# Performance work log

Hardware: AMD Instinct MI355X
Metric: run time of the kernel (lower is better)

The kernel has to match this reference:

```python
import jax, jax.numpy as jnp
import numpy as np

B, T, E, VD, H = 1, 4096, 1024, 2048, 8
KD, HD = E // H, VD // H
EPS = 1e-6


def _make_rel_pos():
    # rotary angles: theta_i = 10000^(-2i/KD), repeated for even/odd pairs
    inv = 1.0 / (10000.0 ** (np.arange(0, KD, 2) / KD))
    angle = np.repeat(inv, 2)[None, :] * np.arange(T)[:, None]  # [T, KD]
    sin = jnp.asarray(np.sin(angle), dtype=jnp.float32)
    cos = jnp.asarray(np.cos(angle), dtype=jnp.float32)
    # per-head causal decay mask: gamma_h^(n-m) for n>=m else 0
    gamma = 1.0 - 2.0 ** (-5.0 - np.arange(H))  # [H]
    n = np.arange(T)
    diff = n[:, None] - n[None, :]  # [T, T]
    logg = np.log(gamma)[:, None, None]
    mask = np.where(diff[None] >= 0, np.exp(logg * np.maximum(diff[None], 0)), 0.0)
    return sin, cos, jnp.asarray(mask, dtype=jnp.float32)


def setup_inputs() -> dict:
    key = jax.random.key(0)
    ks = jax.random.split(key, 6)
    sin, cos, inner_mask = _make_rel_pos()
    s = lambda d: 1.0 / np.sqrt(d)
    return {
        "x": jax.random.normal(ks[0], (B, T, E), dtype=jnp.float32),
        "sin": sin,
        "cos": cos,
        "inner_mask": inner_mask,
        "Wq": jax.random.normal(ks[1], (E, E), dtype=jnp.float32) * s(E),
        "Wk": jax.random.normal(ks[2], (E, E), dtype=jnp.float32) * s(E),
        "Wv": jax.random.normal(ks[3], (E, VD), dtype=jnp.float32) * s(E),
        "Wg": jax.random.normal(ks[4], (E, VD), dtype=jnp.float32) * s(E),
        "Wo": jax.random.normal(ks[5], (VD, E), dtype=jnp.float32) * s(VD),
    }


def _rotate_every_two(x):
    x1 = x[..., ::2]
    x2 = x[..., 1::2]
    return jnp.stack((-x2, x1), axis=-1).reshape(x.shape)


def _theta_shift(x, sin, cos):
    return x * cos + _rotate_every_two(x) * sin


def reference(x, sin, cos, inner_mask, Wq, Wk, Wv, Wg, Wo):
    b, t, e = x.shape
    scaling = KD ** (-0.5)
    q = (x @ Wq).reshape(b, t, H, KD).transpose(0, 2, 1, 3)   # [b,h,t,kd]
    k = (x @ Wk * scaling).reshape(b, t, H, KD).transpose(0, 2, 1, 3)
    v = x @ Wv                                                # [b,t,vd]
    g = x @ Wg                                                # [b,t,vd]
    qr = _theta_shift(q, sin, cos)
    kr = _theta_shift(k, sin, cos)
    vr = v.reshape(b, t, H, HD).transpose(0, 2, 1, 3)         # [b,h,t,hd]
    qk = jnp.einsum('bhtd,bhsd->bhts', qr, kr) * inner_mask   # [b,h,t,t]
    denom = jnp.clip(jnp.abs(jax.lax.stop_gradient(qk)).sum(-1, keepdims=True), 1.0, 50000.0)
    qk = qk / denom
    out = jnp.einsum('bhts,bhsd->bhtd', qk, vr)               # [b,h,t,hd]
    out = out.transpose(0, 2, 1, 3)                           # [b,t,h,hd]
    # RMSNorm over head_dim, no affine
    out = out * jax.lax.rsqrt(jnp.mean(out * out, axis=-1, keepdims=True) + EPS)
    out = out.reshape(b, t, H * HD)
    out = jax.nn.silu(g) * out
    return out @ Wo
```

## Files before the change

kernel.cpp:

```cpp
#include <hip/hip_runtime.h>


typedef __attribute__((ext_vector_type(8)))  short  short8;
typedef __attribute__((ext_vector_type(16))) float  floatx16;

__device__ inline unsigned short f2bf(float f){
  unsigned int u = __builtin_bit_cast(unsigned int, f);
  unsigned int r = (u + 0x7fffu + ((u >> 16) & 1u)) >> 16;
  return (unsigned short)r;
}
__device__ inline float bf2f(unsigned short u){
  unsigned int x = ((unsigned int)u) << 16;
  return __builtin_bit_cast(float, x);
}
__device__ inline void async_cp16(const void* g, const void* l){
  __builtin_amdgcn_global_load_lds((const __attribute__((address_space(1))) void*)g,
                                   (__attribute__((address_space(3))) void*)l, 16, 0, 0);
}

struct us4 { unsigned short a,b,c,d; };
__global__ void k_cvt_x(const float* __restrict__ x, unsigned short* __restrict__ xb, int n4){
  int i = blockIdx.x*blockDim.x + threadIdx.x;
  if (i >= n4) return;
  float4 v = ((const float4*)x)[i];
  us4 o = { f2bf(v.x), f2bf(v.y), f2bf(v.z), f2bf(v.w) };
  ((us4*)xb)[i] = o;
}

struct WPrep  { const float* src; unsigned short* dst; int R; int C; int ntile; };
struct WPrepAll { WPrep w[5]; };
__global__ __launch_bounds__(256) void k_prep_w(WPrepAll a){
  __shared__ float tile[64][65];
  int b = blockIdx.x, i = 0;
  while (b >= a.w[i].ntile){ b -= a.w[i].ntile; ++i; }
  const float* src = a.w[i].src; unsigned short* dst = a.w[i].dst;
  int R = a.w[i].R, C = a.w[i].C;
  int tpr = C >> 6;
  int c0 = (b % tpr)*64, r0 = (b / tpr)*64;
  #pragma unroll
  for (int j=0;j<16;++j){
    int idx = j*256 + threadIdx.x; int r = idx>>6, c = idx&63;
    tile[r][c] = src[(size_t)(r0+r)*C + c0 + c];
  }
  __syncthreads();
  #pragma unroll
  for (int j=0;j<16;++j){
    int idx = j*256 + threadIdx.x; int r = idx>>6, c = idx&63;
    dst[(size_t)(c0+r)*R + r0 + c] = f2bf(tile[c][r]);
  }
}

__global__ __launch_bounds__(256) void k_transpose_b2b(const unsigned short* __restrict__ src,
    unsigned short* __restrict__ dst, int R, int C){
  __shared__ unsigned short tile[64][72];
  int c0 = blockIdx.x*64, r0 = blockIdx.y*64;
  #pragma unroll
  for (int i=0;i<16;++i){
    int idx = i*256 + threadIdx.x; int r = idx>>6, c = idx&63;
    tile[r][c] = src[(size_t)(r0+r)*C + c0 + c];
  }
  __syncthreads();
  #pragma unroll
  for (int i=0;i<16;++i){
    int idx = i*256 + threadIdx.x; int r = idx>>6, c = idx&63;
    dst[(size_t)(c0+r)*R + r0 + c] = tile[c][r];
  }
}

template<int MODE>
__global__ __launch_bounds__(256) void k_gemm_bt(
    const unsigned short* __restrict__ A, const unsigned short* __restrict__ BT,
    int M, int N, int K,
    float* __restrict__ out_f32, unsigned short* __restrict__ out_v,
    unsigned short* __restrict__ out_g)
{
  __shared__ __align__(16) short As[128*64];
  __shared__ __align__(16) short Bs[128*64];
  int bn = blockIdx.x*128, bm = blockIdx.y*128;
  int tid = threadIdx.x;
  int w = tid>>6, l = tid&63;
  int wr = w>>1, wc = w&1;
  int lrow = l&31, lhi = l>>5;
  floatx16 acc[2][2];
  #pragma unroll
  for (int a=0;a<2;++a)
    #pragma unroll
    for (int b=0;b<2;++b)
      #pragma unroll
      for (int j=0;j<16;++j) acc[a][b][j]=0.f;

  int kchunk = K / gridDim.z;
  int k_beg = blockIdx.z * kchunk;
  for (int k0=k_beg; k0<k_beg+kchunk; k0+=64){
    __syncthreads();
    #pragma unroll
    for (int i=0;i<4;++i){
      int idx = i*256 + tid; int r = idx>>3, c = idx&7;
      int cs = c ^ (r&7);
      async_cp16((const char*)A  + ((size_t)(bm+r)*K + k0 + cs*8)*2, &As[idx*8]);
      async_cp16((const char*)BT + ((size_t)(bn+r)*K + k0 + cs*8)*2, &Bs[idx*8]);
    }
    __syncthreads();
    #pragma unroll
    for (int kc=0;kc<4;++kc){
      short8 af[2], bf[2];
      #pragma unroll
      for (int tm=0;tm<2;++tm){
        int row = wr*64 + tm*32 + lrow;
        int pos = (2*kc + lhi) ^ (row&7);
        af[tm] = *(const short8*)&As[row*64 + pos*8];
      }
      #pragma unroll
      for (int tn=0;tn<2;++tn){
        int row = wc*64 + tn*32 + lrow;
        int pos = (2*kc + lhi) ^ (row&7);
        bf[tn] = *(const short8*)&Bs[row*64 + pos*8];
      }
      #pragma unroll
      for (int tm=0;tm<2;++tm)
        #pragma unroll
        for (int tn=0;tn<2;++tn)
          acc[tm][tn] = __builtin_amdgcn_mfma_f32_32x32x16_bf16(af[tm], bf[tn], acc[tm][tn], 0,0,0);
    }
  }
  #pragma unroll
  for (int tm=0;tm<2;++tm)
    #pragma unroll
    for (int tn=0;tn<2;++tn)
      #pragma unroll
      for (int r=0;r<16;++r){
        int row = bm + wr*64 + tm*32 + (r&3) + 8*(r>>2) + 4*lhi;
        int col = bn + wc*64 + tn*32 + lrow;
        float v = acc[tm][tn][r];
        if (MODE==0){
          if (col < 2048)      out_f32[(size_t)row*2048 + col] = v;
          else if (col < 4096) out_v[(size_t)row*2048 + (col-2048)] = f2bf(v);
          else                 out_g[(size_t)row*2048 + (col-4096)] = f2bf(v);
        } else {
          atomicAdd(&out_f32[(size_t)row*N + col], v);
        }
      }
}

__global__ void k_rotary(const float* __restrict__ qk, const float* __restrict__ sinp,
                         const float* __restrict__ cosp,
                         unsigned short* __restrict__ qrp, unsigned short* __restrict__ krp)
{
  int tid = blockIdx.x*blockDim.x + threadIdx.x;
  int t = tid >> 10, p = tid & 1023;
  bool isq = p < 512;
  int c = (isq ? p : p - 512)*2;
  int d = c & 127;
  const float* base = qk + (size_t)t*2048 + (isq ? 0 : 1024) + c;
  float f0 = base[0], f1 = base[1];
  float s0 = sinp[t*128 + d],   s1 = sinp[t*128 + d + 1];
  float c0 = cosp[t*128 + d],   c1 = cosp[t*128 + d + 1];
  float r0 = f0*c0 - f1*s0;
  float r1 = f1*c1 + f0*s1;
  if (!isq){ r0 *= 0.08838834764831845f; r1 *= 0.08838834764831845f; }
  unsigned short* dst = (isq ? qrp : krp) + (size_t)t*1024 + c;
  dst[0] = f2bf(r0); dst[1] = f2bf(r1);
}

__global__ __launch_bounds__(256, 2) void k_attn(
    const unsigned short* __restrict__ qr, const unsigned short* __restrict__ kr,
    const unsigned short* __restrict__ vT,
    unsigned short* __restrict__ o_acc0, unsigned short* __restrict__ o_acc1,
    float* __restrict__ den_g)
{
  int gid = blockIdx.x;
  int head = gid & 7;
  int rest = gid >> 3;
  int qt = 63 - (rest >> 1);
  int chunk = rest & 1;
  int tid = threadIdx.x;
  int w = tid>>6, l = tid&63;
  int qh = w>>1, hh = w&1;
  int lrow = l&31, lhi = l>>5;
  int tbase = qt*64 + qh*32;

  float gamma = 1.f - exp2f(-5.f - (float)head);
  float L = log2f(gamma);

  int dmax = (int)(40.0f/(-L));
  int s_start = tbase - dmax; if (s_start < 0) s_start = 0; s_start &= ~31;
  int N = ((tbase - s_start) >> 5) + 1;
  int half = (N+1)>>1;
  int t0 = chunk ? half : 0;
  int t1 = chunk ? N    : half;

  floatx16 o[4];
  #pragma unroll
  for (int i=0;i<4;++i)
    #pragma unroll
    for (int j=0;j<16;++j) o[i][j]=0.f;
  float den_ = 0.f;

  if (t0 < t1){
    int sb = s_start + t0*32;
    int se = s_start + (t1-1)*32;

    short8 qf[8];
    const unsigned short* qbase = qr + (size_t)(tbase+lrow)*1024 + head*128 + lhi*8;
    #pragma unroll
    for (int kc=0;kc<8;++kc) qf[kc] = *(const short8*)(qbase + kc*16);

    float lanefac = exp2f(L*((float)lrow - 4.0f*(float)lhi));
    float e1[4], e2[4];
    #pragma unroll
    for (int i=0;i<4;++i){ e1[i] = exp2f(-L*(float)i); e2[i] = exp2f(-L*8.0f*(float)i); }

    const unsigned short* kb = kr + head*128 + lhi*8;
    const unsigned short* vb = vT + (size_t)(head*256 + hh*128)*4096 + lhi*8;

#define LOADK(S0, KF) do{ \
    const unsigned short* kp_ = kb + (size_t)((S0)+lrow)*1024; \
    _Pragma("unroll") \
    for (int kc=0;kc<8;++kc) KF[kc] = *(const short8*)(kp_ + kc*16); \
  }while(0)

#define LOADV(S0, VF) do{ \
    const unsigned short* vp_ = vb + (S0); \
    _Pragma("unroll") \
    for (int nt=0;nt<4;++nt){ \
      const unsigned short* vr_ = vp_ + (size_t)(nt*32+lrow)*4096; \
      _Pragma("unroll") \
      for (int kc=0;kc<2;++kc) VF[nt*2+kc] = *(const short8*)(vr_ + kc*16); \
    } \
  }while(0)

#define COMPUTE(S0, KF, VF) do{ \
    floatx16 s_; \
    _Pragma("unroll") for (int j=0;j<16;++j) s_[j]=0.f; \
    __builtin_amdgcn_s_setprio(1); \
    _Pragma("unroll") \
    for (int kc=0;kc<8;++kc) \
      s_ = __builtin_amdgcn_mfma_f32_32x32x16_bf16(KF[kc], qf[kc], s_, 0,0,0); \
    __builtin_amdgcn_s_setprio(0); \
    float tf_ = exp2f(L*(float)(tbase - (S0))) * lanefac; \
    bool diag_ = ((S0) == tbase); \
    float pv_[16]; \
    _Pragma("unroll") \
    for (int r=0;r<16;++r){ \
      float val_ = s_[r]*(tf_*e1[r&3]*e2[r>>2]); \
      if (diag_){ if (lrow < (r&3)+8*(r>>2)+4*lhi) val_ = 0.f; } \
      den_ += fabsf(val_); \
      pv_[r] = val_; \
    } \
    unsigned int w0_,w1_,w2_,w3_,w4_,w5_,w6_,w7_; \
    asm("v_cvt_pk_bf16_f32 %0, %1, %2" : "=v"(w0_) : "v"(pv_[0]),  "v"(pv_[1])); \
    asm("v_cvt_pk_bf16_f32 %0, %1, %2" : "=v"(w1_) : "v"(pv_[2]),  "v"(pv_[3])); \
    asm("v_cvt_pk_bf16_f32 %0, %1, %2" : "=v"(w2_) : "v"(pv_[4]),  "v"(pv_[5])); \
    asm("v_cvt_pk_bf16_f32 %0, %1, %2" : "=v"(w3_) : "v"(pv_[6]),  "v"(pv_[7])); \
    asm("v_cvt_pk_bf16_f32 %0, %1, %2" : "=v"(w4_) : "v"(pv_[8]),  "v"(pv_[9])); \
    asm("v_cvt_pk_bf16_f32 %0, %1, %2" : "=v"(w5_) : "v"(pv_[10]), "v"(pv_[11])); \
    asm("v_cvt_pk_bf16_f32 %0, %1, %2" : "=v"(w6_) : "v"(pv_[12]), "v"(pv_[13])); \
    asm("v_cvt_pk_bf16_f32 %0, %1, %2" : "=v"(w7_) : "v"(pv_[14]), "v"(pv_[15])); \
    asm("v_permlane32_swap_b32 %0, %1" : "+v"(w0_), "+v"(w2_)); \
    asm("v_permlane32_swap_b32 %0, %1" : "+v"(w1_), "+v"(w3_)); \
    asm("v_permlane32_swap_b32 %0, %1" : "+v"(w4_), "+v"(w6_)); \
    asm("v_permlane32_swap_b32 %0, %1" : "+v"(w5_), "+v"(w7_)); \
    union { unsigned int u[4]; short8 s; } pa0_, pa1_; \
    pa0_.u[0]=w0_; pa0_.u[1]=w1_; pa0_.u[2]=w2_; pa0_.u[3]=w3_; \
    pa1_.u[0]=w4_; pa1_.u[1]=w5_; pa1_.u[2]=w6_; pa1_.u[3]=w7_; \
    __builtin_amdgcn_s_setprio(1); \
    _Pragma("unroll") \
    for (int nt=0;nt<4;++nt){ \
      o[nt] = __builtin_amdgcn_mfma_f32_32x32x16_bf16(pa0_.s, VF[nt*2+0], o[nt], 0,0,0); \
      o[nt] = __builtin_amdgcn_mfma_f32_32x32x16_bf16(pa1_.s, VF[nt*2+1], o[nt], 0,0,0); \
    } \
    __builtin_amdgcn_s_setprio(0); \
  }while(0)

    short8 kfA[8], kfB[8];
    LOADK(sb, kfA);
    for (int s0 = sb;; s0 += 64){
      {
        short8 vfA[8];
        LOADV(s0, vfA);
        if (s0 + 32 <= se) LOADK(s0+32, kfB);
        COMPUTE(s0, kfA, vfA);
      }
      if (s0 + 32 > se) break;
      {
        short8 vfB[8];
        LOADV(s0+32, vfB);
        if (s0 + 64 <= se) LOADK(s0+64, kfA);
        COMPUTE(s0+32, kfB, vfB);
      }
      if (s0 + 64 > se) break;
    }
#undef LOADK
#undef LOADV
#undef COMPUTE
  }

  if (hh == 0){
    float d = den_ + __shfl_xor(den_, 32, 64);
    if (lhi == 0)
      den_g[((size_t)chunk*4096 + tbase + lrow)*8 + head] = d;
  }

  unsigned short* ob = chunk ? o_acc1 : o_acc0;
  #pragma unroll
  for (int nt=0;nt<4;++nt)
    #pragma unroll
    for (int r=0;r<16;++r){
      int row = (r&3)+8*(r>>2)+4*lhi;
      ob[(size_t)(tbase+row)*2048 + head*256 + hh*128 + nt*32 + lrow] = f2bf(o[nt][r]);
    }
}

__global__ __launch_bounds__(256) void k_rmsgate(const unsigned short* __restrict__ o_acc0,
    const unsigned short* __restrict__ o_acc1, const unsigned short* __restrict__ g_bf,
    const float* __restrict__ den_g, unsigned short* __restrict__ gated)
{
  int t = blockIdx.x;
  int tid = threadIdx.x;
  int head = tid >> 5;
  float den = den_g[(size_t)t*8 + head] + den_g[(size_t)(4096 + t)*8 + head];
  float rs  = 1.0f/fminf(fmaxf(den, 1.0f), 50000.0f);
  size_t base = (size_t)t*2048 + tid*8;
  short8 av = *(const short8*)(o_acc0 + base);
  short8 bv = *(const short8*)(o_acc1 + base);
  short8 gv = *(const short8*)(g_bf + base);
  float of[8]; float ss = 0.f;
  #pragma unroll
  for (int j=0;j<8;++j){
    of[j] = (bf2f((unsigned short)av[j]) + bf2f((unsigned short)bv[j])) * rs;
    ss += of[j]*of[j];
  }
  #pragma unroll
  for (int off=1; off<32; off<<=1) ss += __shfl_xor(ss, off, 64);
  float rms = rsqrtf(ss*(1.0f/256.0f) + 1e-6f);
  short8 outv;
  #pragma unroll
  for (int j=0;j<8;++j){
    float g = bf2f((unsigned short)gv[j]);
    float si = g / (1.0f + expf(-g));
    outv[j] = (short)f2bf(si * of[j] * rms);
  }
  *(short8*)(gated + base) = outv;
}

extern "C" void kernel_launch(void* const* d_in, const int* in_sizes, int n_in,
                              void* d_out, int out_size, void* d_ws, size_t ws_size,
                              hipStream_t stream)
{
  const float* x    = (const float*)d_in[0];
  const float* sinp = (const float*)d_in[1];
  const float* cosp = (const float*)d_in[2];
  const float* Wq = (const float*)d_in[4];
  const float* Wk = (const float*)d_in[5];
  const float* Wv = (const float*)d_in[6];
  const float* Wg = (const float*)d_in[7];
  const float* Wo = (const float*)d_in[8];

  char* ws = (char*)d_ws;
  size_t off = 0;
  auto alloc = [&](size_t bytes)->char*{ char* p = ws + off; off += (bytes + 255) & ~(size_t)255; return p; };
  unsigned short* x_bf   = (unsigned short*)alloc((size_t)4096*1024*2);
  unsigned short* WallT  = (unsigned short*)alloc((size_t)6144*1024*2);
  float*          qk_f32 = (float*)         alloc((size_t)4096*2048*4);
  unsigned short* v_bf   = (unsigned short*)alloc((size_t)4096*2048*2);
  unsigned short* g_bf   = (unsigned short*)alloc((size_t)4096*2048*2);
  unsigned short* vT     = (unsigned short*)alloc((size_t)2048*4096*2);
  unsigned short* WoT    = (unsigned short*)alloc((size_t)1024*2048*2);
  unsigned short* o_acc1 = (unsigned short*)alloc((size_t)4096*2048*2);
  float*          den_g  = (float*)         alloc((size_t)2*4096*8*4);
  unsigned short* qrp    = x_bf;
  unsigned short* krp    = WallT;
  unsigned short* o_acc0 = (unsigned short*)qk_f32;
  unsigned short* gated  = x_bf;

  hipMemsetAsync(d_out, 0, (size_t)4096*1024*4, stream);

  k_cvt_x<<<4096, 256, 0, stream>>>(x, x_bf, 4096*1024/4);
  WPrepAll pa;
  pa.w[0] = { Wq, WallT,                        1024, 1024, 256 };
  pa.w[1] = { Wk, WallT + 1024*1024,            1024, 1024, 256 };
  pa.w[2] = { Wv, WallT + 2048*1024,            1024, 2048, 512 };
  pa.w[3] = { Wg, WallT + (size_t)4096*1024,    1024, 2048, 512 };
  pa.w[4] = { Wo, WoT,                          2048, 1024, 512 };
  k_prep_w<<<2048, 256, 0, stream>>>(pa);

  k_gemm_bt<0><<<dim3(48,32,1), 256, 0, stream>>>(x_bf, WallT, 4096, 6144, 1024, qk_f32, v_bf, g_bf);

  k_rotary<<<16384, 256, 0, stream>>>(qk_f32, sinp, cosp, qrp, krp);

  k_transpose_b2b<<<dim3(32,64), 256, 0, stream>>>(v_bf, vT, 4096, 2048);

  k_attn<<<1024, 256, 0, stream>>>(qrp, krp, vT, o_acc0, o_acc1, den_g);

  k_rmsgate<<<4096, 256, 0, stream>>>(o_acc0, o_acc1, g_bf, den_g, gated);

  k_gemm_bt<1><<<dim3(8,32,2), 256, 0, stream>>>(gated, WoT, 4096, 1024, 2048,
                                                 (float*)d_out, nullptr, nullptr);

  (void)in_sizes; (void)n_in; (void)out_size; (void)ws_size;
}
```

Measured before the change: 990.3 us.

## Split attention key range into four chunks and replace output atomics with partial-sum reduction

The attention kernel now splits each query tile's key range into four chunks instead of two, doubling the grid to 2048 blocks for more parallelism, and writes four partial outputs and denominators that the RMS/gate kernel sums. The split-K output GEMM writes its two partials to separate buffers, and a new add kernel sums them, replacing atomicAdd and the output memset. Sched barriers are inserted between loads and compute in the attention loop. This costs extra memory traffic for the larger partial buffers and an additional kernel launch.

```diff
diff --git a/kernel.cpp b/kernel.cpp
--- a/kernel.cpp
+++ b/kernel.cpp
@@ -137,9 +137,20 @@
           else if (col < 4096) out_v[(size_t)row*2048 + (col-2048)] = f2bf(v);
           else                 out_g[(size_t)row*2048 + (col-4096)] = f2bf(v);
         } else {
-          atomicAdd(&out_f32[(size_t)row*N + col], v);
+          float* dst = out_f32 + (size_t)blockIdx.z*((size_t)M*N);
+          dst[(size_t)row*N + col] = v;
         }
       }
+}
+
+__global__ void k_addout(const float* __restrict__ p0, const float* __restrict__ p1,
+                         float* __restrict__ out, int n4){
+  int i = blockIdx.x*blockDim.x + threadIdx.x;
+  if (i >= n4) return;
+  float4 a = ((const float4*)p0)[i];
+  float4 b = ((const float4*)p1)[i];
+  float4 o = {a.x+b.x, a.y+b.y, a.z+b.z, a.w+b.w};
+  ((float4*)out)[i] = o;
 }
 
 __global__ void k_rotary(const float* __restrict__ qk, const float* __restrict__ sinp,
@@ -165,14 +176,13 @@
 __global__ __launch_bounds__(256, 2) void k_attn(
     const unsigned short* __restrict__ qr, const unsigned short* __restrict__ kr,
     const unsigned short* __restrict__ vT,
-    unsigned short* __restrict__ o_acc0, unsigned short* __restrict__ o_acc1,
-    float* __restrict__ den_g)
+    unsigned short* __restrict__ o_parts, float* __restrict__ den_g)
 {
   int gid = blockIdx.x;
   int head = gid & 7;
   int rest = gid >> 3;
-  int qt = 63 - (rest >> 1);
-  int chunk = rest & 1;
+  int qt = 63 - (rest >> 2);
+  int chunk = rest & 3;
   int tid = threadIdx.x;
   int w = tid>>6, l = tid&63;
   int qh = w>>1, hh = w&1;
@@ -185,9 +195,9 @@
   int dmax = (int)(40.0f/(-L));
   int s_start = tbase - dmax; if (s_start < 0) s_start = 0; s_start &= ~31;
   int N = ((tbase - s_start) >> 5) + 1;
-  int half = (N+1)>>1;
-  int t0 = chunk ? half : 0;
-  int t1 = chunk ? N    : half;
+  int q4 = (N+3)>>2;
+  int t0 = chunk*q4;
+  int t1 = t0 + q4; if (t1 > N) t1 = N;
 
   floatx16 o[4];
   #pragma unroll
@@ -279,6 +289,7 @@
         short8 vfA[8];
         LOADV(s0, vfA);
         if (s0 + 32 <= se) LOADK(s0+32, kfB);
+        __builtin_amdgcn_sched_barrier(0);
         COMPUTE(s0, kfA, vfA);
       }
       if (s0 + 32 > se) break;
@@ -286,6 +297,7 @@
         short8 vfB[8];
         LOADV(s0+32, vfB);
         if (s0 + 64 <= se) LOADK(s0+64, kfA);
+        __builtin_amdgcn_sched_barrier(0);
         COMPUTE(s0+32, kfB, vfB);
       }
       if (s0 + 64 > se) break;
@@ -301,7 +313,7 @@
       den_g[((size_t)chunk*4096 + tbase + lrow)*8 + head] = d;
   }
 
-  unsigned short* ob = chunk ? o_acc1 : o_acc0;
+  unsigned short* ob = o_parts + (size_t)chunk*4096*2048;
   #pragma unroll
   for (int nt=0;nt<4;++nt)
     #pragma unroll
@@ -311,23 +323,30 @@
     }
 }
 
-__global__ __launch_bounds__(256) void k_rmsgate(const unsigned short* __restrict__ o_acc0,
-    const unsigned short* __restrict__ o_acc1, const unsigned short* __restrict__ g_bf,
-    const float* __restrict__ den_g, unsigned short* __restrict__ gated)
+__global__ __launch_bounds__(256) void k_rmsgate(const unsigned short* __restrict__ o_parts,
+    const unsigned short* __restrict__ g_bf, const float* __restrict__ den_g,
+    unsigned short* __restrict__ gated)
 {
   int t = blockIdx.x;
   int tid = threadIdx.x;
   int head = tid >> 5;
-  float den = den_g[(size_t)t*8 + head] + den_g[(size_t)(4096 + t)*8 + head];
+  float den = den_g[(size_t)t*8 + head]
+            + den_g[(size_t)( 4096 + t)*8 + head]
+            + den_g[(size_t)( 8192 + t)*8 + head]
+            + den_g[(size_t)(12288 + t)*8 + head];
   float rs  = 1.0f/fminf(fmaxf(den, 1.0f), 50000.0f);
   size_t base = (size_t)t*2048 + tid*8;
-  short8 av = *(const short8*)(o_acc0 + base);
-  short8 bv = *(const short8*)(o_acc1 + base);
+  const size_t CS = (size_t)4096*2048;
+  short8 a0 = *(const short8*)(o_parts + base);
+  short8 a1 = *(const short8*)(o_parts + CS + base);
+  short8 a2 = *(const short8*)(o_parts + 2*CS + base);
+  short8 a3 = *(const short8*)(o_parts + 3*CS + base);
   short8 gv = *(const short8*)(g_bf + base);
   float of[8]; float ss = 0.f;
   #pragma unroll
   for (int j=0;j<8;++j){
-    of[j] = (bf2f((unsigned short)av[j]) + bf2f((unsigned short)bv[j])) * rs;
+    of[j] = (bf2f((unsigned short)a0[j]) + bf2f((unsigned short)a1[j])
+           + bf2f((unsigned short)a2[j]) + bf2f((unsigned short)a3[j])) * rs;
     ss += of[j]*of[j];
   }
   #pragma unroll
@@ -366,14 +385,12 @@
   unsigned short* g_bf   = (unsigned short*)alloc((size_t)4096*2048*2);
   unsigned short* vT     = (unsigned short*)alloc((size_t)2048*4096*2);
   unsigned short* WoT    = (unsigned short*)alloc((size_t)1024*2048*2);
-  unsigned short* o_acc1 = (unsigned short*)alloc((size_t)4096*2048*2);
-  float*          den_g  = (float*)         alloc((size_t)2*4096*8*4);
+  unsigned short* o_parts= (unsigned short*)alloc((size_t)4*4096*2048*2);
+  float*          den_g  = (float*)         alloc((size_t)4*4096*8*4);
+  float*          p_out2 = (float*)         alloc((size_t)2*4096*1024*4);
   unsigned short* qrp    = x_bf;
   unsigned short* krp    = WallT;
-  unsigned short* o_acc0 = (unsigned short*)qk_f32;
   unsigned short* gated  = x_bf;
-
-  hipMemsetAsync(d_out, 0, (size_t)4096*1024*4, stream);
 
   k_cvt_x<<<4096, 256, 0, stream>>>(x, x_bf, 4096*1024/4);
   WPrepAll pa;
@@ -390,12 +407,14 @@
 
   k_transpose_b2b<<<dim3(32,64), 256, 0, stream>>>(v_bf, vT, 4096, 2048);
 
-  k_attn<<<1024, 256, 0, stream>>>(qrp, krp, vT, o_acc0, o_acc1, den_g);
-
-  k_rmsgate<<<4096, 256, 0, stream>>>(o_acc0, o_acc1, g_bf, den_g, gated);
+  k_attn<<<2048, 256, 0, stream>>>(qrp, krp, vT, o_parts, den_g);
+
+  k_rmsgate<<<4096, 256, 0, stream>>>(o_parts, g_bf, den_g, gated);
 
   k_gemm_bt<1><<<dim3(8,32,2), 256, 0, stream>>>(gated, WoT, 4096, 1024, 2048,
-                                                 (float*)d_out, nullptr, nullptr);
+                                                 p_out2, nullptr, nullptr);
+  k_addout<<<4096, 256, 0, stream>>>(p_out2, p_out2 + (size_t)4096*1024,
+                                     (float*)d_out, 4096*1024/4);
 
   (void)in_sizes; (void)n_in; (void)out_size; (void)ws_size;
 }
```

Result: no change. 990.0 us, median of 2 (-0.0%).
